# Kernel optimization log

Measured on AMD Instinct MI355X. Metric: run time of the kernel, lower is better.

Reference implementation:

```python
import jax, jax.numpy as jnp
import numpy as np

N_QUBITS = 4
N_LAYERS = 6
BATCH = 262144


def _apply_1q(state, U, wire):
    """Apply a 1-qubit gate U ((2,2) shared or (B,2,2) per-sample) on `wire`.
    state: (B, 2, 2, ..., 2) with n qubit axes after the batch axis."""
    s = jnp.moveaxis(state, 1 + wire, -1)
    shp = s.shape
    s2 = s.reshape(shp[0], -1, 2)
    if U.ndim == 3:
        s2 = jnp.einsum('bij,bkj->bki', U, s2)
    else:
        s2 = jnp.einsum('ij,bkj->bki', U, s2)
    return jnp.moveaxis(s2.reshape(shp), -1, 1 + wire)


def _apply_cnot(state, control, target):
    s = jnp.moveaxis(state, (1 + control, 1 + target), (-2, -1))
    shp = s.shape
    s2 = s.reshape(shp[0], -1, 2, 2)
    # flip target amplitudes where control bit is 1
    s2 = jnp.stack([s2[..., 0, :], s2[..., 1, ::-1]], axis=-2)
    return jnp.moveaxis(s2.reshape(shp), (-2, -1), (1 + control, 1 + target))


def _ry_batched(x):
    """RY(x) for x: (B,) -> (B,2,2) complex64 (real-valued matrix)."""
    c, s = jnp.cos(x / 2), jnp.sin(x / 2)
    m = jnp.stack([jnp.stack([c, -s], -1), jnp.stack([s, c], -1)], -2)
    return m.astype(jnp.complex64)


def _rot(phi, theta, omega):
    """qml.Rot = RZ(omega) RY(theta) RZ(phi), (2,2) complex64."""
    c, s = jnp.cos(theta / 2), jnp.sin(theta / 2)
    e = lambda a: jnp.exp(1j * a)
    m00 = e(-(phi + omega) / 2) * c
    m01 = -e((phi - omega) / 2) * s
    m10 = e(-(phi - omega) / 2) * s
    m11 = e((phi + omega) / 2) * c
    return jnp.stack([jnp.stack([m00, m01]), jnp.stack([m10, m11])]).astype(jnp.complex64)


def setup_inputs() -> dict:
    key = jax.random.key(0)
    k1, k2 = jax.random.split(key)
    inputs = jax.random.normal(k1, (BATCH, N_QUBITS), dtype=jnp.float32)
    quantum_weights = jax.random.uniform(k2, (N_LAYERS, N_QUBITS, 3), dtype=jnp.float32, minval=-0.05, maxval=0.05)
    return {"inputs": inputs, "quantum_weights": quantum_weights}


def reference(inputs, quantum_weights):
    B, n = inputs.shape
    L = quantum_weights.shape[0]
    # |0...0> state, batched
    state = jnp.zeros((B,) + (2,) * n, jnp.complex64)
    state = state.at[(slice(None),) + (0,) * n].set(1.0)
    # AngleEmbedding(rotation='Y'): RY(inputs[:, w]) on wire w
    for w in range(n):
        state = _apply_1q(state, _ry_batched(inputs[:, w]), w)
    # StronglyEntanglingLayers: Rot per wire, then ring of CNOTs with range r = l % (n-1) + 1
    for l in range(L):
        for w in range(n):
            state = _apply_1q(state, _rot(quantum_weights[l, w, 0], quantum_weights[l, w, 1], quantum_weights[l, w, 2]), w)
        r = l % (n - 1) + 1
        for w in range(n):
            state = _apply_cnot(state, w, (w + r) % n)
    # <Z_w> for each wire
    p = jnp.abs(state.reshape(B, -1)) ** 2  # (B, 2^n)
    bits = (jnp.arange(2 ** n)[:, None] >> jnp.arange(n - 1, -1, -1)[None, :]) & 1
    z = (1 - 2 * bits).astype(p.dtype)  # (2^n, n)
    return p @ z  # (B, n) float32
```

## Files before the change

### kernel.cpp

```cpp
#include <hip/hip_runtime.h>

#define N_QUBITS 4
#define N_LAYERS 6
#define NSTATES  16
#define SPT      4

__device__ __forceinline__ float2 cmul(float2 a, float2 b) {
    return make_float2(a.x * b.x - a.y * b.y, a.x * b.y + a.y * b.x);
}
__device__ __forceinline__ float2 cadd(float2 a, float2 b) {
    return make_float2(a.x + b.x, a.y + b.y);
}

__global__ __launch_bounds__(64) void build_u_kernel(
        const float* __restrict__ weights, float* __restrict__ U) {
    __shared__ float2 rotm[N_LAYERS * N_QUBITS][4];

    const int t = threadIdx.x;
    if (t < N_LAYERS * N_QUBITS) {
        const float phi   = weights[t * 3 + 0];
        const float theta = weights[t * 3 + 1];
        const float omega = weights[t * 3 + 2];
        float stheta, ctheta;
        sincosf(theta * 0.5f, &stheta, &ctheta);
        const float a1 = -(phi + omega) * 0.5f;
        const float a2 =  (phi - omega) * 0.5f;
        float s1, c1, s2, c2;
        sincosf(a1, &s1, &c1);
        sincosf(a2, &s2, &c2);
        rotm[t][0] = make_float2( c1 * ctheta,  s1 * ctheta);
        rotm[t][1] = make_float2(-c2 * stheta, -s2 * stheta);
        rotm[t][2] = make_float2( c2 * stheta, -s2 * stheta);
        rotm[t][3] = make_float2( c1 * ctheta, -s1 * ctheta);
    }
    __syncthreads();

    if (t < NSTATES) {
        const int c = t;
        float2 s[NSTATES];
        #pragma unroll
        for (int q = 0; q < NSTATES; ++q)
            s[q] = make_float2(q == c ? 1.0f : 0.0f, 0.0f);

        #pragma unroll
        for (int l = 0; l < N_LAYERS; ++l) {
            #pragma unroll
            for (int w = 0; w < N_QUBITS; ++w) {
                const float2 m00 = rotm[l * N_QUBITS + w][0];
                const float2 m01 = rotm[l * N_QUBITS + w][1];
                const float2 m10 = rotm[l * N_QUBITS + w][2];
                const float2 m11 = rotm[l * N_QUBITS + w][3];
                const int bit = 8 >> w;
                #pragma unroll
                for (int i = 0; i < NSTATES; ++i) {
                    if (i & bit) continue;
                    const int j = i | bit;
                    const float2 a0 = s[i];
                    const float2 a1v = s[j];
                    s[i] = cadd(cmul(m00, a0), cmul(m01, a1v));
                    s[j] = cadd(cmul(m10, a0), cmul(m11, a1v));
                }
            }
            const int r = l % (N_QUBITS - 1) + 1;
            float2 tmp[NSTATES];
            #pragma unroll
            for (int i = 0; i < NSTATES; ++i) {
                int fi = i;
                #pragma unroll
                for (int w = 0; w < N_QUBITS; ++w) {
                    const int tb = 8 >> ((w + r) & 3);
                    if ((fi >> (3 - w)) & 1) fi ^= tb;
                }
                tmp[fi] = s[i];
            }
            #pragma unroll
            for (int i = 0; i < NSTATES; ++i) s[i] = tmp[i];
        }

        #pragma unroll
        for (int i = 0; i < NSTATES; ++i)
            reinterpret_cast<float2*>(U)[i * NSTATES + c] = s[i];
    }
}

template<bool GUARD>
__global__ __launch_bounds__(256) void qc_apply_kernel(
        const float* __restrict__ inputs,
        const float* __restrict__ U,
        float* __restrict__ out,
        int B) {
    const int base = blockIdx.x * (256 * SPT) + threadIdx.x;

    float v[SPT][NSTATES];
    bool live[SPT];
    #pragma unroll
    for (int s = 0; s < SPT; ++s) {
        const int b = base + s * 256;
        live[s] = !GUARD || (b < B);
        const float4 xin = live[s] ? reinterpret_cast<const float4*>(inputs)[b]
                                   : make_float4(0.f, 0.f, 0.f, 0.f);
        float s0, c0, s1, c1, s2, c2, s3, c3;
        __sincosf(xin.x * 0.5f, &s0, &c0);
        __sincosf(xin.y * 0.5f, &s1, &c1);
        __sincosf(xin.z * 0.5f, &s2, &c2);
        __sincosf(xin.w * 0.5f, &s3, &c3);
        const float vA[4] = { c0 * c1, c0 * s1, s0 * c1, s0 * s1 };
        const float vB[4] = { c2 * c3, c2 * s3, s2 * c3, s2 * s3 };
        #pragma unroll
        for (int a = 0; a < 4; ++a)
            #pragma unroll
            for (int q = 0; q < 4; ++q)
                v[s][a * 4 + q] = vA[a] * vB[q];
    }

    float z[SPT][4];
    #pragma unroll
    for (int s = 0; s < SPT; ++s)
        #pragma unroll
        for (int w = 0; w < 4; ++w) z[s][w] = 0.0f;

    #pragma unroll
    for (int i = 0; i < NSTATES; ++i) {
        const float4* row = reinterpret_cast<const float4*>(U + 2 * NSTATES * i);
        float4 u4[8];
        #pragma unroll
        for (int q = 0; q < 8; ++q) u4[q] = row[q];

        #pragma unroll
        for (int s = 0; s < SPT; ++s) {
            float re = 0.0f, im = 0.0f;
            #pragma unroll
            for (int q = 0; q < 8; ++q) {
                re = fmaf(u4[q].x, v[s][2 * q],     re);
                im = fmaf(u4[q].y, v[s][2 * q],     im);
                re = fmaf(u4[q].z, v[s][2 * q + 1], re);
                im = fmaf(u4[q].w, v[s][2 * q + 1], im);
            }
            const float p = re * re + im * im;
            z[s][0] = (i & 8) ? z[s][0] - p : z[s][0] + p;
            z[s][1] = (i & 4) ? z[s][1] - p : z[s][1] + p;
            z[s][2] = (i & 2) ? z[s][2] - p : z[s][2] + p;
            z[s][3] = (i & 1) ? z[s][3] - p : z[s][3] + p;
        }
    }

    #pragma unroll
    for (int s = 0; s < SPT; ++s) {
        const int b = base + s * 256;
        if (!GUARD || live[s])
            reinterpret_cast<float4*>(out)[b] =
                make_float4(z[s][0], z[s][1], z[s][2], z[s][3]);
    }
}

extern "C" void kernel_launch(void* const* d_in, const int* in_sizes, int n_in,
                              void* d_out, int out_size, void* d_ws, size_t ws_size,
                              hipStream_t stream) {
    const float* inputs  = (const float*)d_in[0];
    const float* weights = (const float*)d_in[1];
    float* out = (float*)d_out;
    float* U   = (float*)d_ws;
    const int B = in_sizes[0] / N_QUBITS;

    build_u_kernel<<<1, 64, 0, stream>>>(weights, U);

    const int per_block = 256 * SPT;
    if (B % per_block == 0) {
        qc_apply_kernel<false><<<B / per_block, 256, 0, stream>>>(inputs, U, out, B);
    } else {
        qc_apply_kernel<true><<<(B + per_block - 1) / per_block, 256, 0, stream>>>(inputs, U, out, B);
    }
}
```

Measured before the change: 72.41 us.

## Fuse unitary construction into apply kernel with per-wave LDS copies

```diff
diff --git a/kernel.cpp b/kernel.cpp
--- a/kernel.cpp
+++ b/kernel.cpp
@@ -4,6 +4,24 @@
 #define N_LAYERS 6
 #define NSTATES  16
 #define SPT      4
+#define BLOCK    256
+#define NWAVES   (BLOCK / 64)
+
+struct PermT { int g[3][NSTATES]; };
+constexpr PermT make_perm() {
+    PermT p{};
+    for (int r = 1; r <= 3; ++r)
+        for (int i = 0; i < NSTATES; ++i) {
+            int fi = i;
+            for (int w = 0; w < 4; ++w) {
+                const int tb = 8 >> ((w + r) & 3);
+                if ((fi >> (3 - w)) & 1) fi ^= tb;
+            }
+            p.g[r - 1][fi] = i;
+        }
+    return p;
+}
+__device__ constexpr PermT PERM = make_perm();
 
 __device__ __forceinline__ float2 cmul(float2 a, float2 b) {
     return make_float2(a.x * b.x - a.y * b.y, a.x * b.y + a.y * b.x);
@@ -12,15 +30,23 @@
     return make_float2(a.x + b.x, a.y + b.y);
 }
 
-__global__ __launch_bounds__(64) void build_u_kernel(
-        const float* __restrict__ weights, float* __restrict__ U) {
-    __shared__ float2 rotm[N_LAYERS * N_QUBITS][4];
+template<bool GUARD>
+__global__ __launch_bounds__(BLOCK) void qc_fused_kernel(
+        const float* __restrict__ inputs,
+        const float* __restrict__ weights,
+        float* __restrict__ out,
+        int B) {
+    __shared__ float2 rotm[NWAVES][N_LAYERS * N_QUBITS][4];
+    __shared__ __align__(16) float2 Um[NWAVES][NSTATES][NSTATES];
 
-    const int t = threadIdx.x;
-    if (t < N_LAYERS * N_QUBITS) {
-        const float phi   = weights[t * 3 + 0];
-        const float theta = weights[t * 3 + 1];
-        const float omega = weights[t * 3 + 2];
+    const int tid  = threadIdx.x;
+    const int wv   = tid >> 6;
+    const int lane = tid & 63;
+
+    if (lane < N_LAYERS * N_QUBITS) {
+        const float phi   = weights[lane * 3 + 0];
+        const float theta = weights[lane * 3 + 1];
+        const float omega = weights[lane * 3 + 2];
         float stheta, ctheta;
         sincosf(theta * 0.5f, &stheta, &ctheta);
         const float a1 = -(phi + omega) * 0.5f;
@@ -28,15 +54,14 @@
         float s1, c1, s2, c2;
         sincosf(a1, &s1, &c1);
         sincosf(a2, &s2, &c2);
-        rotm[t][0] = make_float2( c1 * ctheta,  s1 * ctheta);
-        rotm[t][1] = make_float2(-c2 * stheta, -s2 * stheta);
-        rotm[t][2] = make_float2( c2 * stheta, -s2 * stheta);
-        rotm[t][3] = make_float2( c1 * ctheta, -s1 * ctheta);
+        rotm[wv][lane][0] = make_float2( c1 * ctheta,  s1 * ctheta);
+        rotm[wv][lane][1] = make_float2(-c2 * stheta, -s2 * stheta);
+        rotm[wv][lane][2] = make_float2( c2 * stheta, -s2 * stheta);
+        rotm[wv][lane][3] = make_float2( c1 * ctheta, -s1 * ctheta);
     }
-    __syncthreads();
 
-    if (t < NSTATES) {
-        const int c = t;
+    if (lane < NSTATES) {
+        const int c = lane;
         float2 s[NSTATES];
         #pragma unroll
         for (int q = 0; q < NSTATES; ++q)
@@ -46,56 +71,41 @@
         for (int l = 0; l < N_LAYERS; ++l) {
             #pragma unroll
             for (int w = 0; w < N_QUBITS; ++w) {
-                const float2 m00 = rotm[l * N_QUBITS + w][0];
-                const float2 m01 = rotm[l * N_QUBITS + w][1];
-                const float2 m10 = rotm[l * N_QUBITS + w][2];
-                const float2 m11 = rotm[l * N_QUBITS + w][3];
+                const float2 m00 = rotm[wv][l * N_QUBITS + w][0];
+                const float2 m01 = rotm[wv][l * N_QUBITS + w][1];
+                const float2 m10 = rotm[wv][l * N_QUBITS + w][2];
+                const float2 m11 = rotm[wv][l * N_QUBITS + w][3];
                 const int bit = 8 >> w;
                 #pragma unroll
                 for (int i = 0; i < NSTATES; ++i) {
                     if (i & bit) continue;
                     const int j = i | bit;
-                    const float2 a0 = s[i];
+                    const float2 a0  = s[i];
                     const float2 a1v = s[j];
                     s[i] = cadd(cmul(m00, a0), cmul(m01, a1v));
                     s[j] = cadd(cmul(m10, a0), cmul(m11, a1v));
                 }
             }
-            const int r = l % (N_QUBITS - 1) + 1;
-            float2 tmp[NSTATES];
+            const int rr = l % (N_QUBITS - 1);
+            float2 ns[NSTATES];
             #pragma unroll
-            for (int i = 0; i < NSTATES; ++i) {
-                int fi = i;
-                #pragma unroll
-                for (int w = 0; w < N_QUBITS; ++w) {
-                    const int tb = 8 >> ((w + r) & 3);
-                    if ((fi >> (3 - w)) & 1) fi ^= tb;
-                }
-                tmp[fi] = s[i];
-            }
+            for (int j = 0; j < NSTATES; ++j) ns[j] = s[PERM.g[rr][j]];
             #pragma unroll
-            for (int i = 0; i < NSTATES; ++i) s[i] = tmp[i];
+            for (int j = 0; j < NSTATES; ++j) s[j] = ns[j];
         }
 
         #pragma unroll
         for (int i = 0; i < NSTATES; ++i)
-            reinterpret_cast<float2*>(U)[i * NSTATES + c] = s[i];
+            Um[wv][i][c] = s[i];
     }
-}
 
-template<bool GUARD>
-__global__ __launch_bounds__(256) void qc_apply_kernel(
-        const float* __restrict__ inputs,
-        const float* __restrict__ U,
-        float* __restrict__ out,
-        int B) {
-    const int base = blockIdx.x * (256 * SPT) + threadIdx.x;
+    const int base = blockIdx.x * (BLOCK * SPT) + tid;
 
     float v[SPT][NSTATES];
     bool live[SPT];
     #pragma unroll
     for (int s = 0; s < SPT; ++s) {
-        const int b = base + s * 256;
+        const int b = base + s * BLOCK;
         live[s] = !GUARD || (b < B);
         const float4 xin = live[s] ? reinterpret_cast<const float4*>(inputs)[b]
                                    : make_float4(0.f, 0.f, 0.f, 0.f);
@@ -121,7 +131,7 @@
 
     #pragma unroll
     for (int i = 0; i < NSTATES; ++i) {
-        const float4* row = reinterpret_cast<const float4*>(U + 2 * NSTATES * i);
+        const float4* row = reinterpret_cast<const float4*>(&Um[wv][i][0]);
         float4 u4[8];
         #pragma unroll
         for (int q = 0; q < 8; ++q) u4[q] = row[q];
@@ -146,7 +156,7 @@
 
     #pragma unroll
     for (int s = 0; s < SPT; ++s) {
-        const int b = base + s * 256;
+        const int b = base + s * BLOCK;
         if (!GUARD || live[s])
             reinterpret_cast<float4*>(out)[b] =
                 make_float4(z[s][0], z[s][1], z[s][2], z[s][3]);
@@ -159,15 +169,12 @@
     const float* inputs  = (const float*)d_in[0];
     const float* weights = (const float*)d_in[1];
     float* out = (float*)d_out;
-    float* U   = (float*)d_ws;
     const int B = in_sizes[0] / N_QUBITS;
 
-    build_u_kernel<<<1, 64, 0, stream>>>(weights, U);
-
-    const int per_block = 256 * SPT;
+    const int per_block = BLOCK * SPT;
     if (B % per_block == 0) {
-        qc_apply_kernel<false><<<B / per_block, 256, 0, stream>>>(inputs, U, out, B);
+        qc_fused_kernel<false><<<B / per_block, BLOCK, 0, stream>>>(inputs, weights, out, B);
     } else {
-        qc_apply_kernel<true><<<(B + per_block - 1) / per_block, 256, 0, stream>>>(inputs, U, out, B);
+        qc_fused_kernel<true><<<(B + per_block - 1) / per_block, BLOCK, 0, stream>>>(inputs, weights, out, B);
     }
 }
```

Result: faster. 70.05 us (-3.3%).
